# Optimization experiments

Measured on AMD Instinct MI355X. Metric: run time of the kernel, lower is better.

## Reference

```python
import jax, jax.numpy as jnp
import numpy as np

H = 8
HD = 16  # head_dim = out_features // n_heads = 128 // 8


def setup_inputs() -> dict:
    key = jax.random.key(0)
    k1, k2, k3, k4, k5 = jax.random.split(key, 5)
    B, N, F_IN, F_OUT = 4, 2048, 128, 128
    x = jax.random.normal(k1, (B, N, F_IN), dtype=jnp.float32)
    adj = jax.random.randint(k2, (B, N, N), 0, 2, dtype=jnp.int32)
    W = jax.random.normal(k3, (F_IN, F_OUT), dtype=jnp.float32) * (1.0 / np.sqrt(F_IN))
    a = jax.random.normal(k4, (H, 2 * HD), dtype=jnp.float32) * 0.1
    Wo = jax.random.normal(k5, (F_OUT, F_OUT), dtype=jnp.float32) * (1.0 / np.sqrt(F_OUT))
    bo = jnp.zeros((F_OUT,), dtype=jnp.float32)
    return {"x": x, "adj": adj, "W": W, "a": a, "Wo": Wo, "bo": bo}


def reference(x, adj, W, a, Wo, bo):
    B, N, _ = x.shape
    # Linear projection (no bias), split heads: [B,H,N,HD]
    Wx = (x @ W).reshape(B, N, H, HD).transpose(0, 2, 1, 3)
    # Additive attention scores: e_ij = leaky(a_l . Wx_i + a_r . Wx_j)
    e_i = jnp.einsum('bhnd,hd->bhn', Wx, a[:, :HD])  # [B,H,N]
    e_j = jnp.einsum('bhnd,hd->bhn', Wx, a[:, HD:])  # [B,H,N]
    e = jax.nn.leaky_relu(e_i[:, :, :, None] + e_j[:, :, None, :], negative_slope=0.2)
    # Mask to edges of adj; rows with no edges -> all -inf -> softmax NaN -> 0
    mask = (adj[:, None, :, :] == 0)  # [B,1,N,N] broadcast over heads
    e = jnp.where(mask, -jnp.inf, e)
    attn = jax.nn.softmax(e, axis=-1)
    attn = jnp.nan_to_num(attn, nan=0.0)
    # Weighted aggregation, merge heads: [B,N,F_OUT]
    h = jnp.einsum('bhij,bhjd->bhid', attn, Wx)
    h = h.transpose(0, 2, 1, 3).reshape(B, N, H * HD)
    # out_proj (nn.Linear: y = h @ Wo.T + bo) then ELU
    return jax.nn.elu(h @ Wo.T + bo)
```

## Files before the change

kernel.cpp:

```cpp
#include <hip/hip_runtime.h>
#include <hip/hip_bf16.h>
#include <cstdint>


typedef float f32x2 __attribute__((ext_vector_type(2)));
typedef float f32x4 __attribute__((ext_vector_type(4)));
typedef __bf16 bf16x8 __attribute__((ext_vector_type(8)));
typedef unsigned long long u64;

__device__ __forceinline__ float lsel(float v, u64 m, u64 lanebit) {
#if __has_builtin(__builtin_amdgcn_inverse_ballot_w64)
    (void)lanebit;
    return __builtin_amdgcn_inverse_ballot_w64(m) ? v : 0.0f;
#else
    return (m & lanebit) ? v : 0.0f;
#endif
}
__device__ __forceinline__ f32x2 pkmul(f32x2 a, f32x2 b) {
    f32x2 d;
    asm("v_pk_mul_f32 %0, %1, %2" : "=v"(d) : "v"(a), "v"(b));
    return d;
}
__device__ __forceinline__ unsigned cvtpk(float lo, float hi) {
    unsigned d;
    asm("v_cvt_pk_bf16_f32 %0, %1, %2" : "=v"(d) : "v"(lo), "v"(hi));
    return d;
}

__global__ __launch_bounds__(256)
void prep_kernel(const float* __restrict__ x, const float* __restrict__ W,
                 const float* __restrict__ a, const float* __restrict__ Wo,
                 const int* __restrict__ adj,
                 unsigned short* __restrict__ wxT,
                 float2* __restrict__ EI,
                 float* __restrict__ EjT, float* __restrict__ Ej5T,
                 float* __restrict__ WoT,
                 u64* __restrict__ tmask)
{
    const int t = threadIdx.x;

    if (blockIdx.x < 2048) {
        __shared__ int al[16][257];
        const int blk2 = blockIdx.x;
        const int b = blk2 >> 9;
        const int tile = (blk2 >> 2) & 127;
        const int jq = blk2 & 3;
        const int rowbase = b * 2048 + tile * 16;
        const int w = t >> 6, lane = t & 63;
        const int r = lane & 15, jg = lane >> 4;
        const int srow = t >> 4, scol = (t & 15) * 16;

        #pragma unroll
        for (int cc = 0; cc < 2; ++cc) {
            const int jc = jq * 512 + cc * 256;
            const int* gsrc = adj + (size_t)(rowbase + srow) * 2048 + jc + scol;
            #pragma unroll
            for (int q = 0; q < 4; ++q) {
                const int4 v = *reinterpret_cast<const int4*>(&gsrc[q * 4]);
                al[srow][scol + q * 4 + 0] = v.x;
                al[srow][scol + q * 4 + 1] = v.y;
                al[srow][scol + q * 4 + 2] = v.z;
                al[srow][scol + q * 4 + 3] = v.w;
            }
            __syncthreads();
            u64 myw = 0;
            #pragma unroll
            for (int kk = 0; kk < 2; ++kk) {
                const int c0 = w * 64 + kk * 32 + jg * 8;
                const int4 a0 = *reinterpret_cast<const int4*>(&al[r][c0]);
                const int4 a1 = *reinterpret_cast<const int4*>(&al[r][c0 + 4]);
                const int av[8] = {a0.x, a0.y, a0.z, a0.w, a1.x, a1.y, a1.z, a1.w};
                #pragma unroll
                for (int e = 0; e < 8; ++e) {
                    const u64 bal = __ballot(av[e] != 0);
                    const int widx = kk * 8 + e;
                    if (lane == widx) myw = bal;
                }
            }
            __syncthreads();
            const int jtw = jq * 8 + cc * 4 + w;
            if (lane < 16)
                tmask[((size_t)(b * 128 + tile) * 32 + jtw) * 16 + lane] = myw;
        }
        return;
    }

    const int blk = blockIdx.x - 2048;
    if (blk == 1024) {
        if (t < 128)
            for (int k = 0; k < 128; ++k)
                WoT[k * 128 + t] = Wo[t * 128 + k];
        return;
    }
    __shared__ float xl[8 * 128];
    __shared__ float xw[8 * 128];
    const int row0 = blk * 8;
    if (t < 128) {
        #pragma unroll
        for (int r = 0; r < 8; ++r)
            xl[r * 128 + t] = x[(size_t)(row0 + r) * 128 + t];
    }
    __syncthreads();

    if (t < 128) {
        float acc[8] = {0.f, 0.f, 0.f, 0.f, 0.f, 0.f, 0.f, 0.f};
        for (int k = 0; k < 128; k += 4) {
            const float w0 = W[(k + 0) * 128 + t];
            const float w1 = W[(k + 1) * 128 + t];
            const float w2 = W[(k + 2) * 128 + t];
            const float w3 = W[(k + 3) * 128 + t];
            #pragma unroll
            for (int r = 0; r < 8; ++r) {
                const float4 xv = *reinterpret_cast<const float4*>(&xl[r * 128 + k]);
                acc[r] += xv.x * w0 + xv.y * w1 + xv.z * w2 + xv.w * w3;
            }
        }
        #pragma unroll
        for (int r = 0; r < 8; ++r) xw[r * 128 + t] = acc[r];
    }
    __syncthreads();

    if (t < 128) {
        const int b = row0 >> 11, n0 = row0 & 2047;
        bf16x8 st;
        #pragma unroll
        for (int r = 0; r < 8; ++r) st[r] = (__bf16)xw[r * 128 + t];
        *reinterpret_cast<bf16x8*>(&wxT[((size_t)(b * 128 + t)) * 2048 + n0]) = st;

        const int r = t >> 4, h = (t >> 1) & 7, s = t & 1;
        float dot = 0.f;
        #pragma unroll
        for (int d = 0; d < 16; ++d)
            dot += xw[r * 128 + h * 16 + d] * a[h * 32 + s * 16 + d];
        const float ef  = __expf(dot);
        const float ef5 = __expf(0.2f * dot);
        const int idx = (b * 8 + h) * 2048 + n0 + r;
        if (s) { EjT[idx] = ef; Ej5T[idx] = ef5; }
        else   { float2 ev; ev.x = ef; ev.y = ef5; EI[idx] = ev; }
    }
}

__global__ __launch_bounds__(256)
void vshuf_kernel(const unsigned short* __restrict__ wxT,
                  unsigned short* __restrict__ vfrag)
{
    const int gid = blockIdx.x * 256 + threadIdx.x;
    const int lane = gid & 63;
    const int w32 = (gid >> 6) & 63;
    const int bh = gid >> 12;
    const int b = bh >> 3, h = bh & 7;
    const int f = h * 16 + (lane & 15);
    const int j = w32 * 32 + (lane >> 4) * 8;
    const bf16x8 v = *reinterpret_cast<const bf16x8*>(
        &wxT[((size_t)(b * 128 + f)) * 2048 + j]);
    *reinterpret_cast<bf16x8*>(&vfrag[(size_t)gid * 8]) = v;
}

__global__ __launch_bounds__(256, 6)
void gat_part(const u64* __restrict__ tmask,
              const unsigned short* __restrict__ vfrag,
              const float2* __restrict__ EI,
              const float* __restrict__ EjT, const float* __restrict__ Ej5T,
              float* __restrict__ pacc, float* __restrict__ psum)
{
    const int tid = threadIdx.x;
    const int hw = tid >> 6;
    const int lane = tid & 63;
    const int r = lane & 15;
    const int jg = lane >> 4;
    const u64 lanebit = 1ull << lane;
    const int x = blockIdx.x & 7, w = blockIdx.x >> 3;
    const int tg = x * 64 + (w & 63);
    const int sub = w >> 6;
    const int jh = sub >> 1, hg = sub & 1;
    const int b = tg >> 7;
    const int tile = tg & 127;
    const int ibase = tile << 4;
    const int h = hg * 4 + hw;

    __shared__ __align__(16) float EjL[2][4][128];
    __shared__ __align__(16) float Ej5L[2][4][128];

    const int eb = (b * 8 + h) * 2048;
    const float2 q0 = EI[eb + ibase + r];
    f32x2 EiE, Ei5E;
    EiE[0] = q0.x;  EiE[1] = q0.x;
    Ei5E[0] = q0.y; Ei5E[1] = q0.y;
    const u64* tmrow = tmask + (size_t)(b * 128 + tile) * 512;
    const unsigned short* vfr = vfrag + (size_t)(b * 8 + h) * 64 * 64 * 8;
    const float* EjG  = EjT  + eb;
    const float* Ej5G = Ej5T + eb;

    f32x4 acc  = {0.f, 0.f, 0.f, 0.f};
    f32x4 accS = {0.f, 0.f, 0.f, 0.f};
    bf16x8 ones;
    #pragma unroll
    for (int e2 = 0; e2 < 8; ++e2) ones[e2] = (__bf16)1.0f;

    const int jbase = jh * 1024;
    const int wbase = jh * 32;

    bf16x8 vC0, vC1, vC2, vC3, vN0, vN1, vN2, vN3;
    vC0 = *reinterpret_cast<const bf16x8*>(&vfr[((wbase + 0) * 64 + lane) * 8]);
    vC1 = *reinterpret_cast<const bf16x8*>(&vfr[((wbase + 1) * 64 + lane) * 8]);
    vC2 = *reinterpret_cast<const bf16x8*>(&vfr[((wbase + 2) * 64 + lane) * 8]);
    vC3 = *reinterpret_cast<const bf16x8*>(&vfr[((wbase + 3) * 64 + lane) * 8]);
    {
        const float2 s0 = *reinterpret_cast<const float2*>(&EjG[jbase + lane * 2]);
        const float2 s1 = *reinterpret_cast<const float2*>(&Ej5G[jbase + lane * 2]);
        *reinterpret_cast<float2*>(&EjL[0][hw][lane * 2]) = s0;
        *reinterpret_cast<float2*>(&Ej5L[0][hw][lane * 2]) = s1;
    }
    __syncthreads();

    int cur = 0;
    for (int c = 0; c < 8; ++c) {
        const int cn = (c + 1) & 7;
        const int w32n = wbase + cn * 4;
        const int jn = jbase + cn * 128;
        vN0 = *reinterpret_cast<const bf16x8*>(&vfr[((w32n + 0) * 64 + lane) * 8]);
        vN1 = *reinterpret_cast<const bf16x8*>(&vfr[((w32n + 1) * 64 + lane) * 8]);
        vN2 = *reinterpret_cast<const bf16x8*>(&vfr[((w32n + 2) * 64 + lane) * 8]);
        vN3 = *reinterpret_cast<const bf16x8*>(&vfr[((w32n + 3) * 64 + lane) * 8]);
        const float2 sn  = *reinterpret_cast<const float2*>(&EjG[jn + lane * 2]);
        const float2 sn5 = *reinterpret_cast<const float2*>(&Ej5G[jn + lane * 2]);
        __builtin_amdgcn_sched_barrier(0);

        const u64* tmw = tmrow + (jh * 16 + c * 2) * 16;
        u64 mwA[16], mwB[16];
        #pragma unroll
        for (int e2 = 0; e2 < 16; ++e2) mwA[e2] = tmw[e2];
        #pragma unroll
        for (int e2 = 0; e2 < 16; ++e2) mwB[e2] = tmw[16 + e2];

        #pragma unroll
        for (int kk = 0; kk < 4; ++kk) {
            const int jloc = kk * 32 + jg * 8;
            const float4 e0 = *reinterpret_cast<const float4*>(&EjL[cur][hw][jloc]);
            const float4 e1 = *reinterpret_cast<const float4*>(&EjL[cur][hw][jloc + 4]);
            const float4 f0 = *reinterpret_cast<const float4*>(&Ej5L[cur][hw][jloc]);
            const float4 f1 = *reinterpret_cast<const float4*>(&Ej5L[cur][hw][jloc + 4]);
            const bf16x8 v = (kk == 0) ? vC0 : (kk == 1) ? vC1 : (kk == 2) ? vC2 : vC3;
            const u64* mwp = (kk < 2) ? mwA : mwB;
            const int mof = (kk & 1) * 8;
            const float ee[8] = {e0.x, e0.y, e0.z, e0.w, e1.x, e1.y, e1.z, e1.w};
            const float ff[8] = {f0.x, f0.y, f0.z, f0.w, f1.x, f1.y, f1.z, f1.w};
            unsigned au[4];
            #pragma unroll
            for (int q = 0; q < 4; ++q) {
                f32x2 ejp;  ejp[0]  = ee[2 * q]; ejp[1]  = ee[2 * q + 1];
                f32x2 ej5p; ej5p[0] = ff[2 * q]; ej5p[1] = ff[2 * q + 1];
                const f32x2 t1 = pkmul(ejp, EiE);
                const f32x2 t2 = pkmul(ej5p, Ei5E);
                const float m0 = fmaxf(t1[0], t2[0]);
                const float m1 = fmaxf(t1[1], t2[1]);
                const float p0 = lsel(m0, mwp[mof + 2 * q],     lanebit);
                const float p1 = lsel(m1, mwp[mof + 2 * q + 1], lanebit);
                au[q] = cvtpk(p0, p1);
            }
            union { unsigned u[4]; bf16x8 v8; } cvt;
            cvt.u[0] = au[0]; cvt.u[1] = au[1]; cvt.u[2] = au[2]; cvt.u[3] = au[3];
            acc  = __builtin_amdgcn_mfma_f32_16x16x32_bf16(cvt.v8, v,    acc,  0, 0, 0);
            accS = __builtin_amdgcn_mfma_f32_16x16x32_bf16(cvt.v8, ones, accS, 0, 0, 0);
        }

        const int nb = cur ^ 1;
        *reinterpret_cast<float2*>(&EjL[nb][hw][lane * 2]) = sn;
        *reinterpret_cast<float2*>(&Ej5L[nb][hw][lane * 2]) = sn5;
        __syncthreads();
        vC0 = vN0; vC1 = vN1; vC2 = vN2; vC3 = vN3;
        cur = nb;
    }

    const size_t pb = (size_t)((b * 128 + tile) * 2 + jh);
    float* pa = pacc + pb * 2048;
    float* ps = psum + pb * 128;
    #pragma unroll
    for (int q = 0; q < 4; ++q) {
        const int row = jg * 4 + q;
        pa[row * 128 + hg * 64 + hw * 16 + r] = acc[q];
        if (r == 0) ps[(hg * 4 + hw) * 16 + row] = accS[q];
    }
}

__global__ __launch_bounds__(256)
void combine_kernel(const float* __restrict__ pacc, const float* __restrict__ psum,
                    const float* __restrict__ WoT, const float* __restrict__ bo,
                    float* __restrict__ out)
{
    const int tid = threadIdx.x;
    const int bid = (blockIdx.x & 7) * 64 + (blockIdx.x >> 3);
    const int b = bid >> 7;
    const int tile = bid & 127;
    const int ibase = tile << 4;

    __shared__ float hl[16][128];
    const size_t pb0 = (size_t)((b * 128 + tile) * 2);
    const float* pa0 = pacc + pb0 * 2048;
    const float* pa1 = pa0 + 2048;
    const float* ps0 = psum + pb0 * 128;
    const float* ps1 = ps0 + 128;

    #pragma unroll
    for (int k = 0; k < 8; ++k) {
        const int idx = k * 256 + tid;
        const int row = idx >> 7, f = idx & 127, h = f >> 4;
        const float num = pa0[idx] + pa1[idx];
        const float den = ps0[h * 16 + row] + ps1[h * 16 + row];
        const float inv = (den > 0.f) ? 1.f / den : 0.f;
        hl[row][f] = num * inv;
    }
    __syncthreads();

    const int f = tid & 127;
    const int rg = tid >> 7;
    float o[8] = {0.f, 0.f, 0.f, 0.f, 0.f, 0.f, 0.f, 0.f};
    for (int k = 0; k < 128; k += 4) {
        const float w0 = WoT[(k + 0) * 128 + f];
        const float w1 = WoT[(k + 1) * 128 + f];
        const float w2 = WoT[(k + 2) * 128 + f];
        const float w3 = WoT[(k + 3) * 128 + f];
        #pragma unroll
        for (int q = 0; q < 8; ++q) {
            const float4 hv = *reinterpret_cast<const float4*>(&hl[rg * 8 + q][k]);
            o[q] += hv.x * w0 + hv.y * w1 + hv.z * w2 + hv.w * w3;
        }
    }
    const float bv = bo[f];
    #pragma unroll
    for (int q = 0; q < 8; ++q) {
        float v = o[q] + bv;
        v = (v > 0.f) ? v : (__expf(v) - 1.f);
        out[(size_t)(b * 2048 + ibase + rg * 8 + q) * 128 + f] = v;
    }
}

extern "C" void kernel_launch(void* const* d_in, const int* in_sizes, int n_in,
                              void* d_out, int out_size, void* d_ws, size_t ws_size,
                              hipStream_t stream) {
    const float* x   = (const float*)d_in[0];
    const int*   adj = (const int*)d_in[1];
    const float* W   = (const float*)d_in[2];
    const float* a   = (const float*)d_in[3];
    const float* Wo  = (const float*)d_in[4];
    const float* bo  = (const float*)d_in[5];
    float* out = (float*)d_out;

    char* ws = (char*)d_ws;
    unsigned short* wxT = (unsigned short*)ws;
    float2* EI  = (float2*)(ws + (size_t)2 * 1024 * 1024);
    float* EjT  = (float*)(EI + 4 * 8 * 2048);
    float* Ej5T = EjT + 4 * 8 * 2048;
    float* WoT  = Ej5T + 4 * 8 * 2048;
    u64* tmask = (u64*)(WoT + 128 * 128);
    unsigned short* vfrag = (unsigned short*)(tmask + (size_t)512 * 512);
    float* pacc = (float*)(vfrag + (size_t)1024 * 1024);
    float* psum = pacc + (size_t)1024 * 2048;

    prep_kernel<<<dim3(2048 + 1025), dim3(256), 0, stream>>>(
        x, W, a, Wo, adj, wxT, EI, EjT, Ej5T, WoT, tmask);
    vshuf_kernel<<<dim3(512), dim3(256), 0, stream>>>(wxT, vfrag);
    gat_part<<<dim3(2048), dim3(256), 0, stream>>>(
        tmask, vfrag, EI, EjT, Ej5T, pacc, psum);
    combine_kernel<<<dim3(512), dim3(256), 0, stream>>>(
        pacc, psum, WoT, bo, out);
}
```

Measured before the change: 79.56 us.

## Write MFMA-ready V fragments directly from prep and drop vshuf kernel

The prep kernel now stores the projected bf16 features straight into the fragment layout that gat_part consumes, so the separate vshuf_kernel launch and its extra global round trip go away. gat_part's launch bound drops from 6 to 4 waves per SIMD, giving the compiler more registers. The inner loop now loads all Ej/Ej5 LDS values for the four k-steps before the compute loop, which raises register pressure but lets LDS reads overlap with the work. The scattered 16-byte stores from prep may coalesce less well than before.

Result: faster. 72.31 us (-9.1%).

```diff
diff --git a/kernel.cpp b/kernel.cpp
--- a/kernel.cpp
+++ b/kernel.cpp
@@ -31,7 +31,7 @@
 void prep_kernel(const float* __restrict__ x, const float* __restrict__ W,
                  const float* __restrict__ a, const float* __restrict__ Wo,
                  const int* __restrict__ adj,
-                 unsigned short* __restrict__ wxT,
+                 unsigned short* __restrict__ vfrag,
                  float2* __restrict__ EI,
                  float* __restrict__ EjT, float* __restrict__ Ej5T,
                  float* __restrict__ WoT,
@@ -125,7 +125,10 @@
         bf16x8 st;
         #pragma unroll
         for (int r = 0; r < 8; ++r) st[r] = (__bf16)xw[r * 128 + t];
-        *reinterpret_cast<bf16x8*>(&wxT[((size_t)(b * 128 + t)) * 2048 + n0]) = st;
+        const int hh = t >> 4, rr = t & 15;
+        const int w32 = n0 >> 5, jgp = (n0 >> 3) & 3;
+        *reinterpret_cast<bf16x8*>(
+            &vfrag[(((size_t)(b * 8 + hh) * 64 + w32) * 64 + jgp * 16 + rr) * 8]) = st;
 
         const int r = t >> 4, h = (t >> 1) & 7, s = t & 1;
         float dot = 0.f;
@@ -140,23 +143,7 @@
     }
 }
 
-__global__ __launch_bounds__(256)
-void vshuf_kernel(const unsigned short* __restrict__ wxT,
-                  unsigned short* __restrict__ vfrag)
-{
-    const int gid = blockIdx.x * 256 + threadIdx.x;
-    const int lane = gid & 63;
-    const int w32 = (gid >> 6) & 63;
-    const int bh = gid >> 12;
-    const int b = bh >> 3, h = bh & 7;
-    const int f = h * 16 + (lane & 15);
-    const int j = w32 * 32 + (lane >> 4) * 8;
-    const bf16x8 v = *reinterpret_cast<const bf16x8*>(
-        &wxT[((size_t)(b * 128 + f)) * 2048 + j]);
-    *reinterpret_cast<bf16x8*>(&vfrag[(size_t)gid * 8]) = v;
-}
-
-__global__ __launch_bounds__(256, 6)
+__global__ __launch_bounds__(256, 4)
 void gat_part(const u64* __restrict__ tmask,
               const unsigned short* __restrict__ vfrag,
               const float2* __restrict__ EI,
@@ -233,16 +220,22 @@
         #pragma unroll
         for (int e2 = 0; e2 < 16; ++e2) mwB[e2] = tmw[16 + e2];
 
+        float4 E0[4], E1[4], F0[4], F1[4];
         #pragma unroll
         for (int kk = 0; kk < 4; ++kk) {
             const int jloc = kk * 32 + jg * 8;
-            const float4 e0 = *reinterpret_cast<const float4*>(&EjL[cur][hw][jloc]);
-            const float4 e1 = *reinterpret_cast<const float4*>(&EjL[cur][hw][jloc + 4]);
-            const float4 f0 = *reinterpret_cast<const float4*>(&Ej5L[cur][hw][jloc]);
-            const float4 f1 = *reinterpret_cast<const float4*>(&Ej5L[cur][hw][jloc + 4]);
+            E0[kk] = *reinterpret_cast<const float4*>(&EjL[cur][hw][jloc]);
+            E1[kk] = *reinterpret_cast<const float4*>(&EjL[cur][hw][jloc + 4]);
+            F0[kk] = *reinterpret_cast<const float4*>(&Ej5L[cur][hw][jloc]);
+            F1[kk] = *reinterpret_cast<const float4*>(&Ej5L[cur][hw][jloc + 4]);
+        }
+
+        #pragma unroll
+        for (int kk = 0; kk < 4; ++kk) {
             const bf16x8 v = (kk == 0) ? vC0 : (kk == 1) ? vC1 : (kk == 2) ? vC2 : vC3;
             const u64* mwp = (kk < 2) ? mwA : mwB;
             const int mof = (kk & 1) * 8;
+            const float4 e0 = E0[kk], e1 = E1[kk], f0 = F0[kk], f1 = F1[kk];
             const float ee[8] = {e0.x, e0.y, e0.z, e0.w, e1.x, e1.y, e1.z, e1.w};
             const float ff[8] = {f0.x, f0.y, f0.z, f0.w, f1.x, f1.y, f1.z, f1.w};
             unsigned au[4];
@@ -347,19 +340,17 @@
     float* out = (float*)d_out;
 
     char* ws = (char*)d_ws;
-    unsigned short* wxT = (unsigned short*)ws;
+    unsigned short* vfrag = (unsigned short*)ws;
     float2* EI  = (float2*)(ws + (size_t)2 * 1024 * 1024);
     float* EjT  = (float*)(EI + 4 * 8 * 2048);
     float* Ej5T = EjT + 4 * 8 * 2048;
     float* WoT  = Ej5T + 4 * 8 * 2048;
     u64* tmask = (u64*)(WoT + 128 * 128);
-    unsigned short* vfrag = (unsigned short*)(tmask + (size_t)512 * 512);
-    float* pacc = (float*)(vfrag + (size_t)1024 * 1024);
+    float* pacc = (float*)(tmask + (size_t)512 * 512);
     float* psum = pacc + (size_t)1024 * 2048;
 
     prep_kernel<<<dim3(2048 + 1025), dim3(256), 0, stream>>>(
-        x, W, a, Wo, adj, wxT, EI, EjT, Ej5T, WoT, tmask);
-    vshuf_kernel<<<dim3(512), dim3(256), 0, stream>>>(wxT, vfrag);
+        x, W, a, Wo, adj, vfrag, EI, EjT, Ej5T, WoT, tmask);
     gat_part<<<dim3(2048), dim3(256), 0, stream>>>(
         tmask, vfrag, EI, EjT, Ej5T, pacc, psum);
     combine_kernel<<<dim3(512), dim3(256), 0, stream>>>(
```
